# Performance work log

Hardware: AMD Instinct MI355X
Metric: run time of the kernel (lower is better)

## Reference

```python
import jax, jax.numpy as jnp
import numpy as np

EPS = 1e-5  # torch F.instance_norm default eps

def _inorm(x):
    # instance norm over the flattened spatial axis, per (batch, channel)
    m = jnp.mean(x, axis=-1, keepdims=True)
    v = jnp.var(x, axis=-1, keepdims=True)  # biased variance, matches torch
    return (x - m) / jnp.sqrt(v + EPS)

def _conv1x1(x, w, b):
    # x: (b, c, n), w: (o, c), b: (o,) -- Conv1d with kernel_size=1
    return jnp.einsum('bcn,oc->bon', x, w) + b[None, :, None]

def setup_inputs() -> dict:
    key = jax.random.key(0)
    ks = jax.random.split(key, 8)
    B, C, N, M = 4, 256, 4096, 4096
    sc = 1.0 / np.sqrt(C)  # kaiming-ish fan-in scale for 1x1 conv
    return {
        'q': jax.random.normal(ks[0], (B, C, N), jnp.float32),
        'k': jax.random.normal(ks[1], (B, C, M), jnp.float32),
        'w_q': jax.random.normal(ks[2], (C, C), jnp.float32) * sc,
        'b_q': jnp.zeros((C,), jnp.float32),
        'w_k': jax.random.normal(ks[3], (C, C), jnp.float32) * sc,
        'b_k': jnp.zeros((C,), jnp.float32),
        'w_s': jax.random.normal(ks[4], (C, C), jnp.float32) * sc,
        'b_s': jnp.zeros((C,), jnp.float32),
    }

def reference(q, k, w_q, b_q, w_k, b_k, w_s, b_s):
    # c = q, s = k (module aliases them)
    qe = _conv1x1(_inorm(q), w_q, b_q).transpose(0, 2, 1)   # (b, N, C)
    ke = _conv1x1(_inorm(k), w_k, b_k)                      # (b, C, M)
    se = _conv1x1(k, w_s, b_s).transpose(0, 2, 1)           # (b, M, C)
    attn = jax.nn.softmax(jnp.einsum('bnc,bcm->bnm', qe, ke), axis=-1)  # (b, N, M)
    mean = jnp.einsum('bnm,bmc->bnc', attn, se)             # attn-weighted mean
    var = jax.nn.relu(jnp.einsum('bnm,bmc->bnc', attn, se * se) - mean * mean)
    std = jnp.sqrt(var)
    cs = _inorm(q) * std.transpose(0, 2, 1) + mean.transpose(0, 2, 1)  # (b, C, N)
    return cs
```

## Files before the change

kernel.cpp:

```cpp
#include <hip/hip_runtime.h>
#include <hip/hip_bf16.h>
#include <cstdint>

typedef unsigned short u16;
typedef __attribute__((ext_vector_type(8))) _Float16 half8;
typedef __attribute__((ext_vector_type(2))) __fp16 fp16x2;
typedef __attribute__((ext_vector_type(4))) float f32x4;
typedef __attribute__((ext_vector_type(4))) unsigned u32x4;

#define B_ 4
#define C_ 256
#define N_ 4096
#define M_ 4096
#define QB 32
#define KVB 32
#define NT (M_/KVB)
#define LOG2E 1.44269504088896340736f

__device__ __forceinline__ u16 f2h(float x){
  _Float16 h = (_Float16)x;
  return __builtin_bit_cast(u16, h);
}
__device__ __forceinline__ float h2f(u16 h){
  return (float)__builtin_bit_cast(_Float16, h);
}
__device__ __forceinline__ unsigned pkrtz(float a, float b){
  fp16x2 h = __builtin_amdgcn_cvt_pkrtz(a, b);
  return __builtin_bit_cast(unsigned, h);
}
__device__ __forceinline__ float sum2(unsigned w){
  fp16x2 h = __builtin_bit_cast(fp16x2, w);
  return (float)h.x + (float)h.y;
}
__device__ __forceinline__ void gll16(const void* gsrc, void* ldst){
  __builtin_amdgcn_global_load_lds(
      (const __attribute__((address_space(1))) unsigned int*)gsrc,
      (__attribute__((address_space(3))) unsigned int*)ldst, 16, 0, 0);
}
__device__ __forceinline__ void bar_lds(){
  asm volatile("s_waitcnt lgkmcnt(0)" ::: "memory");
  __builtin_amdgcn_s_barrier();
}
__device__ __forceinline__ void sq_hl(half8 v, half8& h2, half8& l2){
  u32x4 vw = __builtin_bit_cast(u32x4, v);
  u32x4 hw, lw;
  #pragma unroll
  for (int j=0;j<4;j++){
    unsigned h, l;
    asm("v_pk_mul_f16 %0, %1, %1" : "=v"(h) : "v"(vw[j]));
    asm("v_pk_fma_f16 %0, %1, %1, %2 neg_lo:[0,0,1] neg_hi:[0,0,1]"
        : "=v"(l) : "v"(vw[j]), "v"(h));
    hw[j] = h; lw[j] = l;
  }
  h2 = __builtin_bit_cast(half8, hw);
  l2 = __builtin_bit_cast(half8, lw);
}

__global__ __launch_bounds__(256) void k_stats(const float* __restrict__ q,
                                               const float* __restrict__ k,
                                               float* __restrict__ sq,
                                               float* __restrict__ sk){
  int row = blockIdx.x;
  const float* src = (row < 1024) ? (q + (size_t)row * N_)
                                  : (k + (size_t)(row - 1024) * N_);
  float s = 0.f, ss = 0.f;
  for (int i = threadIdx.x; i < N_/4; i += 256){
    float4 v = ((const float4*)src)[i];
    s  += v.x + v.y + v.z + v.w;
    ss += v.x*v.x + v.y*v.y + v.z*v.z + v.w*v.w;
  }
  #pragma unroll
  for (int off = 32; off >= 1; off >>= 1){
    s  += __shfl_down(s, off);
    ss += __shfl_down(ss, off);
  }
  __shared__ float rs[4], rss[4];
  int w = threadIdx.x >> 6;
  if ((threadIdx.x & 63) == 0){ rs[w] = s; rss[w] = ss; }
  __syncthreads();
  if (threadIdx.x == 0){
    s  = rs[0]+rs[1]+rs[2]+rs[3];
    ss = rss[0]+rss[1]+rss[2]+rss[3];
    float m   = s * (1.f/N_);
    float var = ss * (1.f/N_) - m*m;
    float r   = rsqrtf(fmaxf(var, 0.f) + 1e-5f);
    float* dst = (row < 1024) ? (sq + row*2) : (sk + (row-1024)*2);
    dst[0] = m; dst[1] = r;
  }
}

__global__ __launch_bounds__(64) void k_wprep(
    const float* __restrict__ wq, const float* __restrict__ bq,
    const float* __restrict__ wk, const float* __restrict__ bk,
    const float* __restrict__ wsw, const float* __restrict__ bs,
    const float* __restrict__ sq, const float* __restrict__ sk,
    u16* __restrict__ wh, u16* __restrict__ wl, float* __restrict__ bias2)
{
  int co = blockIdx.x, z = blockIdx.y;
  int lane = threadIdx.x;
  const float* W; const float* bias; const float* st = nullptr; float sc = 1.f;
  if (z < 4){ W = wq; bias = bq; st = sq + z*512; sc = LOG2E; }
  else if (z < 8){ W = wk; bias = bk; st = sk + (z-4)*512; }
  else { W = wsw; bias = bs; }
  float4 wv = *(const float4*)(W + co*256 + lane*4);
  float w4[4] = {wv.x, wv.y, wv.z, wv.w};
  float vs[4];
  float bsum = 0.f;
  if (st){
    float4 s0 = *(const float4*)(st + lane*8);
    float4 s1 = *(const float4*)(st + lane*8 + 4);
    float mm[4] = {s0.x, s0.z, s1.x, s1.z};
    float rr[4] = {s0.y, s0.w, s1.y, s1.w};
    #pragma unroll
    for (int i=0;i<4;i++){
      vs[i] = w4[i]*rr[i]*sc;
      bsum += w4[i]*rr[i]*mm[i];
    }
  } else {
    #pragma unroll
    for (int i=0;i<4;i++) vs[i] = w4[i];
  }
  u16 hi[4], lo[4];
  #pragma unroll
  for (int i=0;i<4;i++){
    hi[i] = f2h(vs[i]);
    lo[i] = f2h(vs[i] - h2f(hi[i]));
  }
  size_t idx = ((size_t)(z*8 + (lane>>3))*256 + co)*32 + ((lane>>1)&3)*8 + (lane&1)*4;
  *(uint2*)(wh + idx) = make_uint2((unsigned)hi[0] | ((unsigned)hi[1]<<16),
                                   (unsigned)hi[2] | ((unsigned)hi[3]<<16));
  *(uint2*)(wl + idx) = make_uint2((unsigned)lo[0] | ((unsigned)lo[1]<<16),
                                   (unsigned)lo[2] | ((unsigned)lo[3]<<16));
  #pragma unroll
  for (int off = 32; off >= 1; off >>= 1) bsum += __shfl_down(bsum, off);
  if (lane == 0) bias2[z*256 + co] = sc*(bias[co] - bsum);
}

__global__ __launch_bounds__(256, 3) void k_conv(
    const float* __restrict__ q, const float* __restrict__ kk,
    const u16* __restrict__ wh, const u16* __restrict__ wl,
    const float* __restrict__ bias2,
    u16* __restrict__ qe, u16* __restrict__ kt, u16* __restrict__ se)
{
  __shared__ u16 XT[64*256];
  const int tid = threadIdx.x;
  const int spt = blockIdx.x, bz = blockIdx.y;
  const int b = bz / 3, mode = bz - b*3;
  const int sp0 = spt*64;
  const float* X = (mode==0 ? q : kk) + (size_t)b*C_*N_;
  const int z = (mode==0) ? b : (mode==1 ? 4+b : 8);
  const u16* whp = wh + (size_t)z*8*256*32;
  const u16* wlp = wl + (size_t)z*8*256*32;
  const float* bp = bias2 + z*256;

  {
    int kc_l = tid & 15, spq = tid >> 4;
    #pragma unroll
    for (int i=0;i<16;i++){
      int kc = i*16 + kc_l;
      float4 v = *(const float4*)(X + (size_t)kc*N_ + sp0 + spq*4);
      float vv[4] = {v.x, v.y, v.z, v.w};
      #pragma unroll
      for (int e=0;e<4;e++){
        int sp = spq*4 + e;
        int byte = sp*512 + (((kc>>3) ^ (sp&7)) << 4) + (kc&7)*2;
        *(u16*)((char*)XT + byte) = f2h(vv[e]);
      }
    }
  }
  __syncthreads();

  const int wid = tid>>6, lane = tid&63, l15 = lane&15, lg = lane>>4;
  f32x4 acc[4][4];
  #pragma unroll
  for (int i=0;i<4;i++)
    #pragma unroll
    for (int j=0;j<4;j++) acc[i][j] = (f32x4)(0.f);

  #pragma unroll
  for (int ks=0; ks<8; ++ks){
    half8 xf[4];
    #pragma unroll
    for (int st=0; st<4; ++st)
      xf[st] = *(const half8*)((char*)XT + (st*16 + l15)*512 + (((ks*4+lg) ^ (l15&7)) << 4));
    #pragma unroll
    for (int ct=0; ct<4; ++ct){
      size_t woff = ((size_t)(ks*256 + wid*64 + ct*16 + l15))*32 + lg*8;
      half8 bh = *(const half8*)(whp + woff);
      half8 bl = *(const half8*)(wlp + woff);
      #pragma unroll
      for (int st=0; st<4; ++st){
        if (mode < 2){
          acc[st][ct] = __builtin_amdgcn_mfma_f32_16x16x32_f16(xf[st], bh, acc[st][ct], 0,0,0);
          acc[st][ct] = __builtin_amdgcn_mfma_f32_16x16x32_f16(xf[st], bl, acc[st][ct], 0,0,0);
        } else {
          acc[ct][st] = __builtin_amdgcn_mfma_f32_16x16x32_f16(bh, xf[st], acc[ct][st], 0,0,0);
          acc[ct][st] = __builtin_amdgcn_mfma_f32_16x16x32_f16(bl, xf[st], acc[ct][st], 0,0,0);
        }
      }
    }
  }

  if (mode < 2){
    u16* o = (mode==0 ? qe : kt);
    #pragma unroll
    for (int st=0; st<4; ++st){
      #pragma unroll
      for (int ct=0; ct<4; ++ct){
        int co = wid*64 + ct*16 + l15;
        float bb = bp[co];
        #pragma unroll
        for (int r=0;r<4;r++){
          int sp = sp0 + st*16 + lg*4 + r;
          o[(size_t)(b*N_ + sp)*C_ + co] = f2h(acc[st][ct][r] + bb);
        }
      }
    }
  } else {
    #pragma unroll
    for (int ct=0; ct<4; ++ct){
      #pragma unroll
      for (int st=0; st<4; ++st){
        #pragma unroll
        for (int r=0;r<4;r++){
          int co = wid*64 + ct*16 + lg*4 + r;
          float bb = bp[co];
          se[(size_t)(b*C_ + co)*M_ + sp0 + st*16 + l15] = f2h(acc[ct][st][r] + bb);
        }
      }
    }
  }
}

__global__ __launch_bounds__(256, 3) void k_attn(
    const float* __restrict__ q, const float* __restrict__ stq,
    const u16* __restrict__ qe_g, const u16* __restrict__ kt_g,
    const u16* __restrict__ se_g, float* __restrict__ out)
{
  __shared__ u16 KTs[2][KVB*256];
  __shared__ u16 SEL[C_*KVB];
  __shared__ unsigned WTw[QB*16];
  __shared__ float PMX[4][16];
  __shared__ float SRES[QB];
  __shared__ float LRUNS[2][QB];
  __shared__ int FLG[2];

  const int tid = threadIdx.x;
  const int wid = tid >> 6, lane = tid & 63;
  const int l15 = lane & 15, lg = lane >> 4;
  const int qg = wid & 1, mh = wid >> 1;
  const int b = blockIdx.y;
  const int n0 = blockIdx.x * QB;

  half8 qf[8];
  {
    const u16* qb = qe_g + ((size_t)(b*N_ + n0 + qg*16 + l15))*C_;
    #pragma unroll
    for (int ks=0; ks<8; ++ks) qf[ks] = *(const half8*)(qb + ks*32 + lg*8);
  }

  int ktsrc[4], sesrc[4];
  #pragma unroll
  for (int i=0;i<4;i++){
    int g = (i*4 + wid)*64 + lane;
    int row = g >> 5, cin = g & 31;
    ktsrc[i] = row*512 + ((cin ^ (row & 7)) << 4);
    int c = g >> 2, mch = (g & 3) ^ ((c >> 1) & 3);
    sesrc[i] = c*8192 + mch*16;
  }
  const char* ktg = (const char*)kt_g + (size_t)b*M_*512;
  const char* seg = (const char*)se_g + (size_t)b*C_*M_*2;

  float m_run = -1e30f, lrun = 0.f;
  f32x4 accm[2][4], accs[2][4];
  #pragma unroll
  for (int i=0;i<2;i++)
    #pragma unroll
    for (int j=0;j<4;j++){ accm[i][j] = (f32x4)(0.f); accs[i][j] = (f32x4)(0.f); }

  #pragma unroll
  for (int i=0;i<4;i++)
    gll16(ktg + ktsrc[i], (char*)&KTs[0][0] + (i*4 + wid)*1024);

  for (int t=0; t<NT; ++t){
    const int buf = t & 1;
    __syncthreads();

    {
      int soff = t*(KVB*2);
      #pragma unroll
      for (int i=0;i<4;i++)
        gll16(seg + soff + sesrc[i], (char*)&SEL[0] + (i*4 + wid)*1024);
    }
    {
      int tn = (t+1 == NT) ? 0 : t+1;
      int koff = tn*(KVB*512);
      #pragma unroll
      for (int i=0;i<4;i++)
        gll16(ktg + koff + ktsrc[i], (char*)&KTs[buf^1][0] + (i*4 + wid)*1024);
    }

    f32x4 L0 = (f32x4)(0.f);
    {
      const char* ktb = (const char*)&KTs[buf][0];
      int krow = mh*16 + l15;
      __builtin_amdgcn_s_setprio(1);
      #pragma unroll
      for (int ks=0; ks<8; ++ks){
        half8 a0 = *(const half8*)(ktb + krow*512 + (((ks*4 + lg) ^ (l15 & 7)) << 4));
        L0 = __builtin_amdgcn_mfma_f32_16x16x32_f16(a0, qf[ks], L0, 0,0,0);
      }
      __builtin_amdgcn_s_setprio(0);
    }
    float pm = fmaxf(fmaxf(L0[0], L0[1]), fmaxf(L0[2], L0[3]));
    pm = fmaxf(pm, __shfl_xor(pm, 16));
    pm = fmaxf(pm, __shfl_xor(pm, 32));
    if (lg == 0) PMX[wid][l15] = pm;
    bar_lds();

    float m_tile = fmaxf(pm, PMX[wid ^ 2][l15]);
    int flag = __any(m_tile > m_run + 8.0f);
    float sv = 1.0f;
    if (flag){
      float mn = fmaxf(m_run, m_tile);
      sv = exp2f(m_run - mn);
      m_run = mn;
    }
    if (mh == 0 && lg == 0) SRES[qg*16 + l15] = sv;
    if (mh == 0 && lane == 0) FLG[qg] = flag;
    unsigned W0 = pkrtz(exp2f(L0[0]-m_run), exp2f(L0[1]-m_run));
    unsigned W1 = pkrtz(exp2f(L0[2]-m_run), exp2f(L0[3]-m_run));
    {
      int row = qg*16 + l15;
      int c16 = (mh*2 + (lg >> 1)) ^ ((l15 >> 1) & 3);
      *(uint2*)((char*)WTw + row*64 + (c16 << 4) + ((lg & 1) << 3)) = make_uint2(W0, W1);
    }
    float rs = sum2(W0) + sum2(W1);
    rs += __shfl_xor(rs, 16);
    rs += __shfl_xor(rs, 32);
    lrun = lrun * sv + rs;

    asm volatile("s_waitcnt vmcnt(4)" ::: "memory");
    bar_lds();

    if (FLG[0] | FLG[1]){
      #pragma unroll
      for (int rt=0;rt<2;rt++){
        f32x4 s4 = *(const f32x4*)&SRES[rt*16 + lg*4];
        #pragma unroll
        for (int ct=0;ct<4;ct++){
          #pragma unroll
          for (int r=0;r<4;r++){ accm[rt][ct][r] *= s4[r]; accs[rt][ct][r] *= s4[r]; }
        }
      }
    }

    {
      half8 a[2];
      #pragma unroll
      for (int rt=0;rt<2;rt++){
        int row = rt*16 + l15;
        a[rt] = *(const half8*)((char*)WTw + row*64 + ((lg ^ ((l15>>1)&3)) << 4));
      }
      const char* seb = (const char*)&SEL[0];
      #pragma unroll
      for (int ct=0;ct<4;ct++){
        int c = wid*64 + ct*16 + l15;
        half8 v = *(const half8*)(seb + c*64 + ((lg ^ ((c>>1)&3)) << 4));
        half8 h2, l2;
        sq_hl(v, h2, l2);
        __builtin_amdgcn_s_setprio(1);
        #pragma unroll
        for (int rt=0;rt<2;rt++){
          accm[rt][ct] = __builtin_amdgcn_mfma_f32_16x16x32_f16(a[rt], v,  accm[rt][ct], 0,0,0);
          accs[rt][ct] = __builtin_amdgcn_mfma_f32_16x16x32_f16(a[rt], h2, accs[rt][ct], 0,0,0);
          accs[rt][ct] = __builtin_amdgcn_mfma_f32_16x16x32_f16(a[rt], l2, accs[rt][ct], 0,0,0);
        }
        __builtin_amdgcn_s_setprio(0);
      }
    }
  }

  if (lg == 0) LRUNS[mh][qg*16 + l15] = lrun;
  __syncthreads();

  #pragma unroll
  for (int rt=0;rt<2;rt++){
    f32x4 lv0 = *(const f32x4*)&LRUNS[0][rt*16 + lg*4];
    f32x4 lv1 = *(const f32x4*)&LRUNS[1][rt*16 + lg*4];
    f32x4 inv;
    #pragma unroll
    for (int r=0;r<4;r++) inv[r] = 1.f / (lv0[r] + lv1[r]);
    #pragma unroll
    for (int ct=0;ct<4;ct++){
      int c = wid*64 + ct*16 + l15;
      float2 st = *(const float2*)(stq + (size_t)(b*C_ + c)*2);
      size_t base = ((size_t)(b*C_ + c))*(size_t)N_ + (size_t)(n0 + rt*16 + lg*4);
      f32x4 qv = *(const f32x4*)(q + base);
      f32x4 res;
      #pragma unroll
      for (int r=0;r<4;r++){
        float mean = accm[rt][ct][r] * inv[r];
        float ms   = accs[rt][ct][r] * inv[r];
        float sd   = sqrtf(fmaxf(ms - mean*mean, 0.f));
        float qn   = (qv[r] - st.x) * st.y;
        res[r] = qn * sd + mean;
      }
      *(f32x4*)(out + base) = res;
    }
  }
}

extern "C" void kernel_launch(void* const* d_in, const int* in_sizes, int n_in,
                              void* d_out, int out_size, void* d_ws, size_t ws_size,
                              hipStream_t stream){
  const float* q   = (const float*)d_in[0];
  const float* k   = (const float*)d_in[1];
  const float* wq  = (const float*)d_in[2];
  const float* bq  = (const float*)d_in[3];
  const float* wk  = (const float*)d_in[4];
  const float* bk  = (const float*)d_in[5];
  const float* wsw = (const float*)d_in[6];
  const float* bs  = (const float*)d_in[7];
  float* out = (float*)d_out;

  char* w = (char*)d_ws;
  float* stq = (float*)w;
  float* stk = (float*)(w + 8192);
  u16* wh    = (u16*)(w + 16384);
  u16* wl    = (u16*)(w + 16384 + 1179648);
  float* bias2 = (float*)(w + 16384 + 2*1179648);
  char* big  = w + 16384 + 2*1179648 + 16384;
  u16* qe  = (u16*)big;
  u16* kt  = qe + (size_t)B_*N_*C_;
  u16* se  = kt + (size_t)B_*M_*C_;

  k_stats<<<dim3(2048), dim3(256), 0, stream>>>(q, k, stq, stk);
  k_wprep<<<dim3(256, 9), dim3(64), 0, stream>>>(wq, bq, wk, bk, wsw, bs,
                                                 stq, stk, wh, wl, bias2);
  k_conv<<<dim3(64, 12), dim3(256), 0, stream>>>(q, k, wh, wl, bias2, qe, kt, se);
  k_attn<<<dim3(N_/QB, B_), dim3(256), 0, stream>>>(q, stq, qe, kt, se, out);
}
```

Before: 282.7 us.

## Double-buffer SE tiles, compute full QK per wave, swizzle block order

SE value tiles are now double-buffered and prefetched one iteration ahead together with K tiles, instead of being loaded synchronously each iteration. Each wave computes both 16-row halves of the QK logits, which removes the cross-wave max exchange through LDS and one barrier, at the cost of duplicated MFMA work. Block indices are remapped (swizzled) across batches, and the occupancy target is lowered to 2 blocks to fit the larger LDS footprint. The explicit vmcnt wait is removed, which relies on barriers to ensure prefetched LDS data is ready.

```diff
diff --git a/kernel.cpp b/kernel.cpp
--- a/kernel.cpp
+++ b/kernel.cpp
@@ -232,15 +232,14 @@
   }
 }
 
-__global__ __launch_bounds__(256, 3) void k_attn(
+__global__ __launch_bounds__(256, 2) void k_attn(
     const float* __restrict__ q, const float* __restrict__ stq,
     const u16* __restrict__ qe_g, const u16* __restrict__ kt_g,
     const u16* __restrict__ se_g, float* __restrict__ out)
 {
   __shared__ u16 KTs[2][KVB*256];
-  __shared__ u16 SEL[C_*KVB];
+  __shared__ u16 SEs[2][C_*KVB];
   __shared__ unsigned WTw[QB*16];
-  __shared__ float PMX[4][16];
   __shared__ float SRES[QB];
   __shared__ float LRUNS[2][QB];
   __shared__ int FLG[2];
@@ -249,8 +248,10 @@
   const int wid = tid >> 6, lane = tid & 63;
   const int l15 = lane & 15, lg = lane >> 4;
   const int qg = wid & 1, mh = wid >> 1;
-  const int b = blockIdx.y;
-  const int n0 = blockIdx.x * QB;
+  const int wg = blockIdx.x + (int)gridDim.x * blockIdx.y;
+  const int sw = (wg & 7)*64 + (wg >> 3);
+  const int b = sw >> 7;
+  const int n0 = (sw & 127) * QB;
 
   half8 qf[8];
   {
@@ -279,57 +280,58 @@
     for (int j=0;j<4;j++){ accm[i][j] = (f32x4)(0.f); accs[i][j] = (f32x4)(0.f); }
 
   #pragma unroll
-  for (int i=0;i<4;i++)
-    gll16(ktg + ktsrc[i], (char*)&KTs[0][0] + (i*4 + wid)*1024);
+  for (int i=0;i<4;i++){
+    int o = (i*4 + wid)*1024;
+    gll16(ktg + ktsrc[i], (char*)&KTs[0][0] + o);
+    gll16(seg + sesrc[i], (char*)&SEs[0][0] + o);
+  }
 
   for (int t=0; t<NT; ++t){
     const int buf = t & 1;
     __syncthreads();
 
-    {
-      int soff = t*(KVB*2);
-      #pragma unroll
-      for (int i=0;i<4;i++)
-        gll16(seg + soff + sesrc[i], (char*)&SEL[0] + (i*4 + wid)*1024);
-    }
-    {
-      int tn = (t+1 == NT) ? 0 : t+1;
-      int koff = tn*(KVB*512);
-      #pragma unroll
-      for (int i=0;i<4;i++)
-        gll16(ktg + koff + ktsrc[i], (char*)&KTs[buf^1][0] + (i*4 + wid)*1024);
-    }
-
-    f32x4 L0 = (f32x4)(0.f);
+    if (t+1 < NT){
+      const int nb = buf ^ 1;
+      int koff = (t+1)*(KVB*512);
+      int soff = (t+1)*(KVB*2);
+      #pragma unroll
+      for (int i=0;i<4;i++){
+        int o = (i*4 + wid)*1024;
+        gll16(ktg + koff + ktsrc[i], (char*)&KTs[nb][0] + o);
+        gll16(seg + soff + sesrc[i], (char*)&SEs[nb][0] + o);
+      }
+    }
+
+    f32x4 L0 = (f32x4)(0.f), L1 = (f32x4)(0.f);
     {
       const char* ktb = (const char*)&KTs[buf][0];
-      int krow = mh*16 + l15;
       __builtin_amdgcn_s_setprio(1);
       #pragma unroll
       for (int ks=0; ks<8; ++ks){
-        half8 a0 = *(const half8*)(ktb + krow*512 + (((ks*4 + lg) ^ (l15 & 7)) << 4));
+        int ch = ((ks*4 + lg) ^ (l15 & 7)) << 4;
+        half8 a0 = *(const half8*)(ktb + l15*512 + ch);
+        half8 a1 = *(const half8*)(ktb + (16+l15)*512 + ch);
         L0 = __builtin_amdgcn_mfma_f32_16x16x32_f16(a0, qf[ks], L0, 0,0,0);
+        L1 = __builtin_amdgcn_mfma_f32_16x16x32_f16(a1, qf[ks], L1, 0,0,0);
       }
       __builtin_amdgcn_s_setprio(0);
     }
-    float pm = fmaxf(fmaxf(L0[0], L0[1]), fmaxf(L0[2], L0[3]));
+    float pm = fmaxf(fmaxf(fmaxf(L0[0],L0[1]), fmaxf(L0[2],L0[3])),
+                     fmaxf(fmaxf(L1[0],L1[1]), fmaxf(L1[2],L1[3])));
     pm = fmaxf(pm, __shfl_xor(pm, 16));
     pm = fmaxf(pm, __shfl_xor(pm, 32));
-    if (lg == 0) PMX[wid][l15] = pm;
-    bar_lds();
-
-    float m_tile = fmaxf(pm, PMX[wid ^ 2][l15]);
-    int flag = __any(m_tile > m_run + 8.0f);
+    int flag = __any(pm > m_run + 8.0f);
     float sv = 1.0f;
     if (flag){
-      float mn = fmaxf(m_run, m_tile);
+      float mn = fmaxf(m_run, pm);
       sv = exp2f(m_run - mn);
       m_run = mn;
     }
     if (mh == 0 && lg == 0) SRES[qg*16 + l15] = sv;
     if (mh == 0 && lane == 0) FLG[qg] = flag;
-    unsigned W0 = pkrtz(exp2f(L0[0]-m_run), exp2f(L0[1]-m_run));
-    unsigned W1 = pkrtz(exp2f(L0[2]-m_run), exp2f(L0[3]-m_run));
+    f32x4 Lm = mh ? L1 : L0;
+    unsigned W0 = pkrtz(exp2f(Lm[0]-m_run), exp2f(Lm[1]-m_run));
+    unsigned W1 = pkrtz(exp2f(Lm[2]-m_run), exp2f(Lm[3]-m_run));
     {
       int row = qg*16 + l15;
       int c16 = (mh*2 + (lg >> 1)) ^ ((l15 >> 1) & 3);
@@ -339,8 +341,6 @@
     rs += __shfl_xor(rs, 16);
     rs += __shfl_xor(rs, 32);
     lrun = lrun * sv + rs;
-
-    asm volatile("s_waitcnt vmcnt(4)" ::: "memory");
     bar_lds();
 
     if (FLG[0] | FLG[1]){
@@ -362,7 +362,7 @@
         int row = rt*16 + l15;
         a[rt] = *(const half8*)((char*)WTw + row*64 + ((lg ^ ((l15>>1)&3)) << 4));
       }
-      const char* seb = (const char*)&SEL[0];
+      const char* seb = (const char*)&SEs[buf][0];
       #pragma unroll
       for (int ct=0;ct<4;ct++){
         int c = wid*64 + ct*16 + l15;
```

Measured after the change: 263.4 us. 1.07x faster.

## Split attention over two KV halves with a separate combine kernel

Applied to the files above, without the earlier changes.

The attention kernel now splits the KV sequence into two halves, giving 1024 workgroups instead of 512 so more blocks are available to fill the GPU. Each half writes normalized partial mean, E[s^2] and (max, sum) statistics to workspace. A new combine kernel merges the two halves with softmax rescaling and applies the instance-norm output. This adds extra global memory traffic for the partials and one more kernel launch.

```diff
diff --git a/kernel.cpp b/kernel.cpp
--- a/kernel.cpp
+++ b/kernel.cpp
@@ -14,7 +14,7 @@
 #define M_ 4096
 #define QB 32
 #define KVB 32
-#define NT (M_/KVB)
+#define NT 64
 #define LOG2E 1.44269504088896340736f
 
 __device__ __forceinline__ u16 f2h(float x){
@@ -233,9 +233,10 @@
 }
 
 __global__ __launch_bounds__(256, 3) void k_attn(
-    const float* __restrict__ q, const float* __restrict__ stq,
     const u16* __restrict__ qe_g, const u16* __restrict__ kt_g,
-    const u16* __restrict__ se_g, float* __restrict__ out)
+    const u16* __restrict__ se_g,
+    float* __restrict__ pmean, float* __restrict__ pEs,
+    float2* __restrict__ pml)
 {
   __shared__ u16 KTs[2][KVB*256];
   __shared__ u16 SEL[C_*KVB];
@@ -243,14 +244,18 @@
   __shared__ float PMX[4][16];
   __shared__ float SRES[QB];
   __shared__ float LRUNS[2][QB];
+  __shared__ float MRS[QB];
   __shared__ int FLG[2];
 
   const int tid = threadIdx.x;
   const int wid = tid >> 6, lane = tid & 63;
   const int l15 = lane & 15, lg = lane >> 4;
   const int qg = wid & 1, mh = wid >> 1;
-  const int b = blockIdx.y;
-  const int n0 = blockIdx.x * QB;
+  const int wg = blockIdx.x;
+  const int y = wg & 7, n0t = wg >> 3;
+  const int b = y >> 1, half = y & 1;
+  const int n0 = n0t * QB;
+  const int pidx = y*128 + n0t;
 
   half8 qf[8];
   {
@@ -266,9 +271,9 @@
     int row = g >> 5, cin = g & 31;
     ktsrc[i] = row*512 + ((cin ^ (row & 7)) << 4);
     int c = g >> 2, mch = (g & 3) ^ ((c >> 1) & 3);
-    sesrc[i] = c*8192 + mch*16;
-  }
-  const char* ktg = (const char*)kt_g + (size_t)b*M_*512;
+    sesrc[i] = c*8192 + half*4096 + mch*16;
+  }
+  const char* ktg = (const char*)kt_g + (size_t)b*M_*512 + (size_t)half*2048*512;
   const char* seg = (const char*)se_g + (size_t)b*C_*M_*2;
 
   float m_run = -1e30f, lrun = 0.f;
@@ -287,17 +292,16 @@
     __syncthreads();
 
     {
-      int soff = t*(KVB*2);
+      int soff = t*64;
       #pragma unroll
       for (int i=0;i<4;i++)
         gll16(seg + soff + sesrc[i], (char*)&SEL[0] + (i*4 + wid)*1024);
     }
     {
-      int tn = (t+1 == NT) ? 0 : t+1;
-      int koff = tn*(KVB*512);
+      int tn = (t+1 < NT) ? t+1 : t;
       #pragma unroll
       for (int i=0;i<4;i++)
-        gll16(ktg + koff + ktsrc[i], (char*)&KTs[buf^1][0] + (i*4 + wid)*1024);
+        gll16(ktg + tn*16384 + ktsrc[i], (char*)&KTs[buf^1][0] + (i*4 + wid)*1024);
     }
 
     f32x4 L0 = (f32x4)(0.f);
@@ -382,8 +386,13 @@
   }
 
   if (lg == 0) LRUNS[mh][qg*16 + l15] = lrun;
+  if (mh == 0 && lg == 0) MRS[qg*16 + l15] = m_run;
   __syncthreads();
 
+  if (tid < QB){
+    float lt = LRUNS[0][tid] + LRUNS[1][tid];
+    pml[(size_t)pidx*QB + tid] = make_float2(MRS[tid], lt);
+  }
   #pragma unroll
   for (int rt=0;rt<2;rt++){
     f32x4 lv0 = *(const f32x4*)&LRUNS[0][rt*16 + lg*4];
@@ -394,20 +403,55 @@
     #pragma unroll
     for (int ct=0;ct<4;ct++){
       int c = wid*64 + ct*16 + l15;
-      float2 st = *(const float2*)(stq + (size_t)(b*C_ + c)*2);
-      size_t base = ((size_t)(b*C_ + c))*(size_t)N_ + (size_t)(n0 + rt*16 + lg*4);
-      f32x4 qv = *(const f32x4*)(q + base);
-      f32x4 res;
+      size_t base = (size_t)pidx*8192 + c*32 + rt*16 + lg*4;
+      f32x4 vm, vs;
       #pragma unroll
       for (int r=0;r<4;r++){
-        float mean = accm[rt][ct][r] * inv[r];
-        float ms   = accs[rt][ct][r] * inv[r];
-        float sd   = sqrtf(fmaxf(ms - mean*mean, 0.f));
-        float qn   = (qv[r] - st.x) * st.y;
-        res[r] = qn * sd + mean;
-      }
-      *(f32x4*)(out + base) = res;
-    }
+        vm[r] = accm[rt][ct][r] * inv[r];
+        vs[r] = accs[rt][ct][r] * inv[r];
+      }
+      *(f32x4*)(pmean + base) = vm;
+      *(f32x4*)(pEs   + base) = vs;
+    }
+  }
+}
+
+__global__ __launch_bounds__(256) void k_comb(
+    const float* __restrict__ q, const float* __restrict__ stq,
+    const float* __restrict__ pmean, const float* __restrict__ pEs,
+    const float2* __restrict__ pml, float* __restrict__ out)
+{
+  const int n0t = blockIdx.x, b = blockIdx.y;
+  const int pA = (b*2 + 0)*128 + n0t;
+  const int pB = pA + 128;
+  const int tid = threadIdx.x, wid = tid >> 6, lane = tid & 63;
+  const int hw = lane >> 5, qr = lane & 31;
+  const int n0 = n0t * QB;
+
+  float2 A = pml[(size_t)pA*QB + qr];
+  float2 Bp = pml[(size_t)pB*QB + qr];
+  float m  = fmaxf(A.x, Bp.x);
+  float wA = A.y * exp2f(A.x - m);
+  float wB = Bp.y * exp2f(Bp.x - m);
+  float inv = 1.f / (wA + wB);
+  float al = wA * inv, be = wB * inv;
+
+  const float* mA = pmean + (size_t)pA*8192;
+  const float* mB = pmean + (size_t)pB*8192;
+  const float* sA = pEs   + (size_t)pA*8192;
+  const float* sB = pEs   + (size_t)pB*8192;
+
+  #pragma unroll 4
+  for (int i=0;i<32;i++){
+    int c = i*8 + wid*2 + hw;
+    int off = c*32 + qr;
+    float mean = al*mA[off] + be*mB[off];
+    float Es   = al*sA[off] + be*sB[off];
+    float sd   = sqrtf(fmaxf(Es - mean*mean, 0.f));
+    float2 st  = *(const float2*)(stq + (size_t)(b*C_ + c)*2);
+    size_t gx  = ((size_t)(b*C_ + c))*(size_t)N_ + n0 + qr;
+    float qn   = (q[gx] - st.x) * st.y;
+    out[gx] = qn * sd + mean;
   }
 }
 
@@ -434,10 +478,14 @@
   u16* qe  = (u16*)big;
   u16* kt  = qe + (size_t)B_*N_*C_;
   u16* se  = kt + (size_t)B_*M_*C_;
+  float* pmean = (float*)(se + (size_t)B_*M_*C_);
+  float* pEs   = pmean + (size_t)1024*8192;
+  float2* pml  = (float2*)(pEs + (size_t)1024*8192);
 
   k_stats<<<dim3(2048), dim3(256), 0, stream>>>(q, k, stq, stk);
   k_wprep<<<dim3(256, 9), dim3(64), 0, stream>>>(wq, bq, wk, bk, wsw, bs,
                                                  stq, stk, wh, wl, bias2);
   k_conv<<<dim3(64, 12), dim3(256), 0, stream>>>(q, k, wh, wl, bias2, qe, kt, se);
-  k_attn<<<dim3(N_/QB, B_), dim3(256), 0, stream>>>(q, stq, qe, kt, se, out);
-}
+  k_attn<<<dim3(1024), dim3(256), 0, stream>>>(qe, kt, se, pmean, pEs, pml);
+  k_comb<<<dim3(128, B_), dim3(256), 0, stream>>>(q, stq, pmean, pEs, pml, out);
+}
```

Result: slower. 297.3 us (+5.2%).
